# Optimization experiments

Hardware: AMD Instinct MI355X
Metric: run time of the kernel (lower is better)

Reference implementation:

```python
import jax, jax.numpy as jnp
import numpy as np


def setup_inputs() -> dict:
    key = jax.random.key(0)
    k1, k2 = jax.random.split(key)
    B, N, F, K = 8, 8192, 128, 512
    x = jax.random.normal(k1, (B, N, F), dtype=jnp.float32)
    cluster_centers = jax.random.normal(k2, (K, F), dtype=jnp.float32)
    return {"x": x, "cluster_centers": cluster_centers}


def reference(x, cluster_centers):
    # same math as sqrt(sum((x - c)^2)) without the [B,N,K,F] intermediate).
    x_sq = jnp.sum(x * x, axis=-1, keepdims=True)                 # [B, N, 1]
    c_sq = jnp.sum(cluster_centers * cluster_centers, axis=-1)    # [K]
    cross = jnp.einsum("bnf,kf->bnk", x, cluster_centers)         # [B, N, K]
    d2 = jnp.maximum(x_sq + c_sq[None, None, :] - 2.0 * cross, 0.0)
    distances = jnp.sqrt(d2)                                      # [B, N, K]
    associations = jax.nn.softmax(-distances, axis=-1)            # [B, N, K]
    output = jnp.einsum("bnk,kf->bnf", associations, cluster_centers)
    return output
```

## Files before the change

kernel.cpp:

```cpp
#include <hip/hip_runtime.h>
#include <hip/hip_bf16.h>

typedef short v8s __attribute__((ext_vector_type(8)));
typedef float v16f __attribute__((ext_vector_type(16)));
typedef unsigned v2u __attribute__((ext_vector_type(2)));

#define F_ 128
#define K_ 512
#define M_ 65536
#define CH_SH 17408
#define CB_OFF 9216

typedef __attribute__((address_space(1))) const char gch;
typedef __attribute__((address_space(3))) char lch;

__device__ __forceinline__ short f2bf(float f) {
    union { float f; unsigned u; } v; v.f = f;
    unsigned u = v.u;
    u = (u + 0x7FFFu + ((u >> 16) & 1u)) >> 16;
    return (short)u;
}
__device__ __forceinline__ float bf2f(short s) {
    union { float f; unsigned u; } v;
    v.u = ((unsigned)(unsigned short)s) << 16;
    return v.f;
}

#if __has_builtin(__builtin_amdgcn_permlane32_swap)
#define HAVE_PLS 1
#endif

__device__ __forceinline__ void pswap(unsigned &a, unsigned &b, int lane) {
#ifdef HAVE_PLS
    v2u r = __builtin_amdgcn_permlane32_swap(a, b, false, false);
    a = (unsigned)r.x; b = (unsigned)r.y;
#else
    unsigned sa = (unsigned)__shfl_xor((int)a, 32);
    unsigned sb = (unsigned)__shfl_xor((int)b, 32);
    if (lane & 32) a = sb; else b = sa;
#endif
}

__global__ void prep_kernel(const float* __restrict__ centers, short* __restrict__ G) {
    const int c = blockIdx.x;
    const int f = threadIdx.x;
    const int ch = c >> 6, c64 = c & 63;
    const size_t base = (size_t)ch * CH_SH;
    float v = centers[c * F_ + f];
    short b = f2bf(v);
    float vb = bf2f(b);
    { const int ks = f >> 4, h = (f >> 3) & 1, j = f & 7;
      G[base + (size_t)((ks * 2 + h) * 64 + c64) * 8 + j] = b; }
    { const int kap = c64 >> 4, hh = (c64 >> 3) & 1, jj = c64 & 7;
      G[base + CB_OFF + (size_t)((kap * 2 + hh) * F_ + f) * 8 + jj] = b; }
    float s = vb * vb;
    #pragma unroll
    for (int off = 1; off < 64; off <<= 1) s += __shfl_xor(s, off);
    __shared__ float part[2];
    if ((f & 63) == 0) part[f >> 6] = s;
    __syncthreads();
    if (f < 16) {
        const float csq = part[0] + part[1];
        const float chv = -0.5f * csq;
        const short vh = f2bf(chv);
        const short vl = f2bf(chv - bf2f(vh));
        const short val = (f == 0) ? vh : (f == 1) ? vl : (f == 2) ? (short)0x3F80 : (short)0;
        const int h2 = f >> 3, j2 = f & 7;
        G[base + (size_t)((16 + h2) * 64 + c64) * 8 + j2] = val;
    }
}

__device__ __forceinline__ void stage_chunk(const short* __restrict__ G, short* dst,
                                            int ch, int wave, int lane) {
    const char* src = (const char*)(G + (size_t)ch * CH_SH);
    lch* d = (lch*)dst;
    #pragma unroll
    for (int t = 0; t < 8; ++t) {
        const int g = t * 256 + wave * 64 + lane;
        __builtin_amdgcn_global_load_lds((gch*)(src + (size_t)g * 16),
                                         d + (size_t)(t * 256 + wave * 64) * 16, 16, 0, 0);
    }
    if (wave < 2) {
        const int g = 2048 + wave * 64 + lane;
        __builtin_amdgcn_global_load_lds((gch*)(src + (size_t)g * 16),
                                         d + (size_t)(2048 + wave * 64) * 16, 16, 0, 0);
    }
}

__global__ __launch_bounds__(256, 2) void cluster_kernel(
        const float* __restrict__ x, const short* __restrict__ G,
        float* __restrict__ out) {
    __shared__ __align__(16) short SB[2][CH_SH];
    const int tid = threadIdx.x;
    const int wave = tid >> 6, lane = tid & 63;
    const int h = lane >> 5, c32 = lane & 31;
    const int row0 = blockIdx.x * 128 + wave * 32;

    const float4* xr4 = (const float4*)(x + (size_t)(row0 + c32) * F_);
    float4 xl[16];
    #pragma unroll
    for (int ks = 0; ks < 8; ++ks) {
        xl[2 * ks]     = xr4[ks * 4 + h * 2];
        xl[2 * ks + 1] = xr4[ks * 4 + h * 2 + 1];
    }
    v8s Bx[9];
    float xs = 0.f;
    #pragma unroll
    for (int ks = 0; ks < 8; ++ks) {
        float vv[8] = {xl[2*ks].x, xl[2*ks].y, xl[2*ks].z, xl[2*ks].w,
                       xl[2*ks+1].x, xl[2*ks+1].y, xl[2*ks+1].z, xl[2*ks+1].w};
        v8s fr;
        #pragma unroll
        for (int j = 0; j < 8; ++j) {
            short bb = f2bf(vv[j]);
            fr[j] = bb;
            float r = bf2f(bb);
            xs += r * r;
        }
        Bx[ks] = fr;
    }
    xs += __shfl_xor(xs, 32);
    {
        const float xh = -0.5f * xs;
        const short sxh = f2bf(xh);
        const short sxl = f2bf(xh - bf2f(sxh));
        v8s e = (v8s){0, 0, 0, 0, 0, 0, 0, 0};
        if (h == 0) { e[0] = (short)0x3F80; e[1] = (short)0x3F80; e[2] = sxh; e[3] = sxl; }
        Bx[8] = e;
    }

    v16f Of[4];
    #pragma unroll
    for (int ft = 0; ft < 4; ++ft)
        #pragma unroll
        for (int e2 = 0; e2 < 16; ++e2) Of[ft][e2] = 0.f;
    float lden = 0.f;

    stage_chunk(G, SB[0], blockIdx.x & 7, wave, lane);
    asm volatile("s_waitcnt vmcnt(0)" ::: "memory");
    __syncthreads();

    #pragma unroll 2
    for (int i = 0; i < 8; ++i) {
        const short* CbS = SB[i & 1];
        const short* CTS = CbS + CB_OFF;
        if (i < 7) stage_chunk(G, SB[(i + 1) & 1], (i + 1 + blockIdx.x) & 7, wave, lane);

        v16f a0, a1;
        #pragma unroll
        for (int e2 = 0; e2 < 16; ++e2) { a0[e2] = 0.f; a1[e2] = 0.f; }
        {
            v8s f0a = *(const v8s*)&CbS[(size_t)((0 * 2 + h) * 64 + c32) * 8];
            v8s f1a = *(const v8s*)&CbS[(size_t)((0 * 2 + h) * 64 + 32 + c32) * 8];
            v8s f0b = *(const v8s*)&CbS[(size_t)((1 * 2 + h) * 64 + c32) * 8];
            v8s f1b = *(const v8s*)&CbS[(size_t)((1 * 2 + h) * 64 + 32 + c32) * 8];
            #pragma unroll
            for (int ks = 0; ks < 9; ++ks) {
                v8s c0 = f0a, c1 = f1a;
                f0a = f0b; f1a = f1b;
                if (ks < 7) {
                    f0b = *(const v8s*)&CbS[(size_t)(((ks + 2) * 2 + h) * 64 + c32) * 8];
                    f1b = *(const v8s*)&CbS[(size_t)(((ks + 2) * 2 + h) * 64 + 32 + c32) * 8];
                }
                a0 = __builtin_amdgcn_mfma_f32_32x32x16_bf16(c0, Bx[ks], a0, 0, 0, 0);
                a1 = __builtin_amdgcn_mfma_f32_32x32x16_bf16(c1, Bx[ks], a1, 0, 0, 0);
            }
        }

        #pragma unroll
        for (int ct = 0; ct < 2; ++ct) {
            v8s cf[8];
            #pragma unroll
            for (int kp = 0; kp < 2; ++kp)
                #pragma unroll
                for (int ft = 0; ft < 4; ++ft)
                    cf[kp * 4 + ft] = *(const v8s*)
                        &CTS[(size_t)(((ct * 2 + kp) * 2 + h) * F_ + ft * 32 + c32) * 8];
            const v16f acc = ct ? a1 : a0;
            unsigned U[8];
            #pragma unroll
            for (int t = 0; t < 8; ++t) {
                const float d20 = fmaxf(-2.0f * acc[2 * t], 0.f);
                const float d21 = fmaxf(-2.0f * acc[2 * t + 1], 0.f);
                const float p0 = __expf(-__builtin_amdgcn_sqrtf(d20));
                const float p1 = __expf(-__builtin_amdgcn_sqrtf(d21));
                union { __hip_bfloat162 hh; unsigned u; } cv;
                cv.hh = __float22bfloat162_rn(make_float2(p0, p1));
                U[t] = cv.u;
                lden += __uint_as_float(cv.u << 16);
                lden += __uint_as_float(cv.u & 0xffff0000u);
            }
            #pragma unroll
            for (int kp = 0; kp < 2; ++kp) {
                unsigned s0 = U[4 * kp],     s2 = U[4 * kp + 2];
                unsigned s1 = U[4 * kp + 1], s3 = U[4 * kp + 3];
                pswap(s0, s2, lane);
                pswap(s1, s3, lane);
                union { v8s v; unsigned u[4]; } pf;
                pf.u[0] = s0; pf.u[1] = s1; pf.u[2] = s2; pf.u[3] = s3;
                #pragma unroll
                for (int ft = 0; ft < 4; ++ft)
                    Of[ft] = __builtin_amdgcn_mfma_f32_32x32x16_bf16(pf.v, cf[kp * 4 + ft], Of[ft], 0, 0, 0);
            }
        }
        asm volatile("s_waitcnt vmcnt(0)" ::: "memory");
        __syncthreads();
    }

    lden += __shfl_xor(lden, 32);
    const float inv = 1.0f / lden;
    float invr[16];
    #pragma unroll
    for (int r = 0; r < 16; ++r)
        invr[r] = __shfl(inv, (r & 3) + 8 * (r >> 2) + 4 * h);
    #pragma unroll
    for (int ft = 0; ft < 4; ++ft)
        #pragma unroll
        for (int r = 0; r < 16; ++r) {
            const int xrow = (r & 3) + 8 * (r >> 2) + 4 * h;
            out[(size_t)(row0 + xrow) * F_ + ft * 32 + c32] = Of[ft][r] * invr[r];
        }
}

extern "C" void kernel_launch(void* const* d_in, const int* in_sizes, int n_in,
                              void* d_out, int out_size, void* d_ws, size_t ws_size,
                              hipStream_t stream) {
    const float* x       = (const float*)d_in[0];
    const float* centers = (const float*)d_in[1];
    float* out = (float*)d_out;
    short* G = (short*)d_ws;
    prep_kernel<<<K_, F_, 0, stream>>>(centers, G);
    cluster_kernel<<<M_ / 128, 256, 0, stream>>>(x, G, out);
}
```

Baseline: 103.6 us.

## Read center fragments directly from global memory instead of staging in LDS

Removes the double-buffered LDS staging of center chunks via global_load_lds along with the per-iteration barriers. Each wave now loads its MFMA operand fragments straight from global memory (L2/L1 cached), and the chunk loop is no longer unrolled. This frees LDS and drops the block-level synchronisation, but every wave now issues its own global loads with higher latency and no cross-wave sharing, which could stall the MFMA chain.

```diff
diff --git a/kernel.cpp b/kernel.cpp
--- a/kernel.cpp
+++ b/kernel.cpp
@@ -10,9 +10,6 @@
 #define M_ 65536
 #define CH_SH 17408
 #define CB_OFF 9216
-
-typedef __attribute__((address_space(1))) const char gch;
-typedef __attribute__((address_space(3))) char lch;
 
 __device__ __forceinline__ short f2bf(float f) {
     union { float f; unsigned u; } v; v.f = f;
@@ -70,31 +67,13 @@
     }
 }
 
-__device__ __forceinline__ void stage_chunk(const short* __restrict__ G, short* dst,
-                                            int ch, int wave, int lane) {
-    const char* src = (const char*)(G + (size_t)ch * CH_SH);
-    lch* d = (lch*)dst;
-    #pragma unroll
-    for (int t = 0; t < 8; ++t) {
-        const int g = t * 256 + wave * 64 + lane;
-        __builtin_amdgcn_global_load_lds((gch*)(src + (size_t)g * 16),
-                                         d + (size_t)(t * 256 + wave * 64) * 16, 16, 0, 0);
-    }
-    if (wave < 2) {
-        const int g = 2048 + wave * 64 + lane;
-        __builtin_amdgcn_global_load_lds((gch*)(src + (size_t)g * 16),
-                                         d + (size_t)(2048 + wave * 64) * 16, 16, 0, 0);
-    }
-}
-
 __global__ __launch_bounds__(256, 2) void cluster_kernel(
         const float* __restrict__ x, const short* __restrict__ G,
         float* __restrict__ out) {
-    __shared__ __align__(16) short SB[2][CH_SH];
     const int tid = threadIdx.x;
-    const int wave = tid >> 6, lane = tid & 63;
+    const int lane = tid & 63;
     const int h = lane >> 5, c32 = lane & 31;
-    const int row0 = blockIdx.x * 128 + wave * 32;
+    const int row0 = blockIdx.x * 128 + (tid >> 6) * 32;
 
     const float4* xr4 = (const float4*)(x + (size_t)(row0 + c32) * F_);
     float4 xl[16];
@@ -136,31 +115,26 @@
         for (int e2 = 0; e2 < 16; ++e2) Of[ft][e2] = 0.f;
     float lden = 0.f;
 
-    stage_chunk(G, SB[0], blockIdx.x & 7, wave, lane);
-    asm volatile("s_waitcnt vmcnt(0)" ::: "memory");
-    __syncthreads();
-
-    #pragma unroll 2
-    for (int i = 0; i < 8; ++i) {
-        const short* CbS = SB[i & 1];
-        const short* CTS = CbS + CB_OFF;
-        if (i < 7) stage_chunk(G, SB[(i + 1) & 1], (i + 1 + blockIdx.x) & 7, wave, lane);
+    #pragma unroll 1
+    for (int j = 0; j < 8; ++j) {
+        const short* CbG = G + (size_t)(((j + blockIdx.x) & 7)) * CH_SH;
+        const short* CTG = CbG + CB_OFF;
 
         v16f a0, a1;
         #pragma unroll
         for (int e2 = 0; e2 < 16; ++e2) { a0[e2] = 0.f; a1[e2] = 0.f; }
         {
-            v8s f0a = *(const v8s*)&CbS[(size_t)((0 * 2 + h) * 64 + c32) * 8];
-            v8s f1a = *(const v8s*)&CbS[(size_t)((0 * 2 + h) * 64 + 32 + c32) * 8];
-            v8s f0b = *(const v8s*)&CbS[(size_t)((1 * 2 + h) * 64 + c32) * 8];
-            v8s f1b = *(const v8s*)&CbS[(size_t)((1 * 2 + h) * 64 + 32 + c32) * 8];
+            v8s f0a = *(const v8s*)&CbG[(size_t)((0 * 2 + h) * 64 + c32) * 8];
+            v8s f1a = *(const v8s*)&CbG[(size_t)((0 * 2 + h) * 64 + 32 + c32) * 8];
+            v8s f0b = *(const v8s*)&CbG[(size_t)((1 * 2 + h) * 64 + c32) * 8];
+            v8s f1b = *(const v8s*)&CbG[(size_t)((1 * 2 + h) * 64 + 32 + c32) * 8];
             #pragma unroll
             for (int ks = 0; ks < 9; ++ks) {
                 v8s c0 = f0a, c1 = f1a;
                 f0a = f0b; f1a = f1b;
                 if (ks < 7) {
-                    f0b = *(const v8s*)&CbS[(size_t)(((ks + 2) * 2 + h) * 64 + c32) * 8];
-                    f1b = *(const v8s*)&CbS[(size_t)(((ks + 2) * 2 + h) * 64 + 32 + c32) * 8];
+                    f0b = *(const v8s*)&CbG[(size_t)(((ks + 2) * 2 + h) * 64 + c32) * 8];
+                    f1b = *(const v8s*)&CbG[(size_t)(((ks + 2) * 2 + h) * 64 + 32 + c32) * 8];
                 }
                 a0 = __builtin_amdgcn_mfma_f32_32x32x16_bf16(c0, Bx[ks], a0, 0, 0, 0);
                 a1 = __builtin_amdgcn_mfma_f32_32x32x16_bf16(c1, Bx[ks], a1, 0, 0, 0);
@@ -175,7 +149,7 @@
                 #pragma unroll
                 for (int ft = 0; ft < 4; ++ft)
                     cf[kp * 4 + ft] = *(const v8s*)
-                        &CTS[(size_t)(((ct * 2 + kp) * 2 + h) * F_ + ft * 32 + c32) * 8];
+                        &CTG[(size_t)(((ct * 2 + kp) * 2 + h) * F_ + ft * 32 + c32) * 8];
             const v16f acc = ct ? a1 : a0;
             unsigned U[8];
             #pragma unroll
@@ -203,8 +177,6 @@
                     Of[ft] = __builtin_amdgcn_mfma_f32_32x32x16_bf16(pf.v, cf[kp * 4 + ft], Of[ft], 0, 0, 0);
             }
         }
-        asm volatile("s_waitcnt vmcnt(0)" ::: "memory");
-        __syncthreads();
     }
 
     lden += __shfl_xor(lden, 32);
```

Result: slower. 142.3 us (+37.4%).
